# Kernel tuning notes

Hardware: AMD Instinct MI355X
Metric: run time of the kernel (lower is better)

The kernel has to match this reference:

```python
import jax, jax.numpy as jnp
import numpy as np

N = 50000      # nodes
E = 800000     # edges
IN = 256       # in_channels
OUT = 128      # out_channels
HID = 2 * OUT  # hidden = 2*out_channels


def setup_inputs() -> dict:
    key = jax.random.key(0)
    ks = jax.random.split(key, 8)
    x = jax.random.normal(ks[0], (N, IN), dtype=jnp.float32)
    edge_index = jax.random.randint(ks[1], (2, E), 0, N, dtype=jnp.int32)
    def glorot(k, fan_in, fan_out):
        return jax.random.normal(k, (fan_in, fan_out), jnp.float32) * np.float32(1.0 / np.sqrt(fan_in))
    W1 = glorot(ks[2], IN, HID)
    b1 = jnp.zeros((HID,), jnp.float32)
    Wmu = glorot(ks[3], HID, OUT)
    bmu = jnp.zeros((OUT,), jnp.float32)
    Wls = glorot(ks[4], HID, OUT)
    bls = jnp.zeros((OUT,), jnp.float32)
    return {"x": x, "edge_index": edge_index, "W1": W1, "b1": b1,
            "Wmu": Wmu, "bmu": bmu, "Wls": Wls, "bls": bls}


def reference(x, edge_index, W1, b1, Wmu, bmu, Wls, bls):
    n = x.shape[0]
    # add self-loops (PyG GCNConv default add_self_loops=True)
    loop = jnp.arange(n, dtype=edge_index.dtype)
    src = jnp.concatenate([edge_index[0], loop])  # message sources (row)
    dst = jnp.concatenate([edge_index[1], loop])  # aggregation targets (col)
    # symmetric normalization: deg over targets, norm = d^-1/2[src] * d^-1/2[dst]
    deg = jax.ops.segment_sum(jnp.ones(src.shape[0], x.dtype), dst, num_segments=n)
    dinv = jnp.where(deg > 0, jax.lax.rsqrt(deg), 0.0)
    norm = dinv[src] * dinv[dst]  # [E+N]

    def gcn(h, W, b):
        h = h @ W                                   # [N, F_out] dense transform
        msg = h[src] * norm[:, None]                # gather + scale   [E+N, F_out]
        agg = jax.ops.segment_sum(msg, dst, num_segments=n)  # scatter-add
        return agg + b

    h = jax.nn.relu(gcn(x, W1, b1))
    return gcn(h, Wmu, bmu), gcn(h, Wls, bls)
```

## Files before the change

### kernel.cpp

```cpp
#include <hip/hip_runtime.h>
#include <hip/hip_fp16.h>

typedef __attribute__((ext_vector_type(8))) _Float16 half8;
typedef __attribute__((ext_vector_type(4))) _Float16 half4;
typedef __attribute__((ext_vector_type(4))) float float4v;

#define LDP2 72


__global__ __launch_bounds__(256) void k_deg(const int* __restrict__ dst, int* __restrict__ deg, int E) {
    int e = blockIdx.x * 256 + threadIdx.x;
    if (e < E) atomicAdd(&deg[dst[e]], 1);
}


__global__ __launch_bounds__(256) void k_scan1(const int* __restrict__ deg, int* __restrict__ rowptr,
                                               int* __restrict__ bsum, float* __restrict__ dinv, int N) {
    __shared__ int sm[256];
    const int t = threadIdx.x;
    const int i = blockIdx.x * 256 + t;
    int v = (i < N) ? deg[i] : 0;
    if (i < N) dinv[i] = rsqrtf((float)(v + 1));
    int x = v;
    sm[t] = x;
    __syncthreads();
#pragma unroll
    for (int off = 1; off < 256; off <<= 1) {
        int y = (t >= off) ? sm[t - off] : 0;
        __syncthreads();
        x += y;
        sm[t] = x;
        __syncthreads();
    }
    if (i < N) rowptr[i] = x - v;
    if (t == 255) bsum[blockIdx.x] = x;
}

__global__ __launch_bounds__(256) void k_scan2(int* __restrict__ bsum, int* __restrict__ rowptr, int nb, int N) {
    __shared__ int sm[256];
    const int t = threadIdx.x;
    int v = (t < nb) ? bsum[t] : 0;
    int x = v;
    sm[t] = x;
    __syncthreads();
#pragma unroll
    for (int off = 1; off < 256; off <<= 1) {
        int y = (t >= off) ? sm[t - off] : 0;
        __syncthreads();
        x += y;
        sm[t] = x;
        __syncthreads();
    }
    if (t < nb) bsum[t] = x - v;
    if (t == 255) rowptr[N] = x;
}

__global__ __launch_bounds__(256) void k_scan3(int* __restrict__ rowptr, const int* __restrict__ bsum, int N) {
    int i = blockIdx.x * 256 + threadIdx.x;
    if (i < N) rowptr[i] += bsum[blockIdx.x];
}

__global__ __launch_bounds__(256) void k_fill(const int* __restrict__ src, const int* __restrict__ dst,
                                              const int* __restrict__ rowptr, int* __restrict__ rowcnt,
                                              int* __restrict__ csr, int E) {
    int e = blockIdx.x * 256 + threadIdx.x;
    if (e < E) {
        int d = dst[e];
        int pos = rowptr[d] + atomicAdd(&rowcnt[d], 1);
        csr[pos] = src[e];
    }
}

__global__ __launch_bounds__(256) void k_wt(const float* __restrict__ W1, const float* __restrict__ Wmu,
                                            const float* __restrict__ Wls, _Float16* __restrict__ Wt1,
                                            _Float16* __restrict__ Wct) {
    int b = blockIdx.x;
    int t = threadIdx.x;
    if (b < 256) {
        Wt1[b * 256 + t] = (_Float16)W1[t * 256 + b];
    } else {
        int j = b - 256;
        float v = (j < 128) ? Wmu[t * 128 + j] : Wls[t * 128 + (j - 128)];
        Wct[j * 256 + t] = (_Float16)v;
    }
}

template <int AF32, int OUTF32>
__global__ __launch_bounds__(256) void gemm_k(const void* __restrict__ Aptr, const _Float16* __restrict__ Bt,
                                              const float* __restrict__ bmu, const float* __restrict__ bls,
                                              const float* __restrict__ dinv,
                                              void* __restrict__ outp, int M, size_t split) {
    __shared__ _Float16 As[128 * LDP2];
    __shared__ _Float16 Bs[128 * LDP2];
    const int t = threadIdx.x;
    const int lane = t & 63;
    const int wid = t >> 6;
    const int bm = blockIdx.x * 128;
    const int bn = blockIdx.y * 128;
    const int wm = (wid & 1) * 64;
    const int wn = (wid >> 1) * 64;

    float4v acc[4][4];
#pragma unroll
    for (int i = 0; i < 4; i++)
#pragma unroll
        for (int j = 0; j < 4; j++) acc[i][j] = (float4v){0.f, 0.f, 0.f, 0.f};

    float4v ar32[8];
    half8 ar16[4];
    half8 br[4];

    const int a32row = t >> 1;
    const int a32ko = (t & 1) * 32;

    auto load_regs = [&](int kt) {
        if (AF32) {
            const float* A = (const float*)Aptr;
            int gr = bm + a32row; if (gr >= M) gr = M - 1;
            const float4v* p = (const float4v*)(A + (size_t)gr * 256 + kt + a32ko);
#pragma unroll
            for (int q = 0; q < 8; q++) ar32[q] = p[q];
        } else {
            const _Float16* A = (const _Float16*)Aptr;
#pragma unroll
            for (int m = 0; m < 4; m++) {
                int u = m * 256 + t;
                int row = u >> 3, k8 = (u & 7) * 8;
                int gr = bm + row; if (gr >= M) gr = M - 1;
                ar16[m] = *(const half8*)(A + (size_t)gr * 256 + kt + k8);
            }
        }
#pragma unroll
        for (int m = 0; m < 4; m++) {
            int u = m * 256 + t;
            int row = u >> 3, k8 = (u & 7) * 8;
            br[m] = *(const half8*)(Bt + (size_t)(bn + row) * 256 + kt + k8);
        }
    };

    auto write_lds = [&]() {
        if (AF32) {
#pragma unroll
            for (int q = 0; q < 4; q++) {
                half8 h;
#pragma unroll
                for (int j = 0; j < 4; j++) { h[j] = (_Float16)ar32[2 * q][j]; h[4 + j] = (_Float16)ar32[2 * q + 1][j]; }
                *(half8*)&As[a32row * LDP2 + a32ko + q * 8] = h;
            }
        } else {
#pragma unroll
            for (int m = 0; m < 4; m++) {
                int u = m * 256 + t;
                int row = u >> 3, k8 = (u & 7) * 8;
                *(half8*)&As[row * LDP2 + k8] = ar16[m];
            }
        }
#pragma unroll
        for (int m = 0; m < 4; m++) {
            int u = m * 256 + t;
            int row = u >> 3, k8 = (u & 7) * 8;
            *(half8*)&Bs[row * LDP2 + k8] = br[m];
        }
    };

    load_regs(0);
#pragma unroll
    for (int it = 0; it < 4; it++) {
        if (it > 0) __syncthreads();
        write_lds();
        __syncthreads();
        if (it < 3) load_regs((it + 1) * 64);

        const int kg = (lane >> 4) * 8;
        const int fr = lane & 15;
#pragma unroll
        for (int kk = 0; kk < 64; kk += 32) {
            half8 af[4], bf[4];
#pragma unroll
            for (int f = 0; f < 4; f++) af[f] = *(const half8*)&As[(wm + f * 16 + fr) * LDP2 + kk + kg];
#pragma unroll
            for (int f = 0; f < 4; f++) bf[f] = *(const half8*)&Bs[(wn + f * 16 + fr) * LDP2 + kk + kg];
#pragma unroll
            for (int i = 0; i < 4; i++)
#pragma unroll
                for (int j = 0; j < 4; j++)
                    acc[i][j] = __builtin_amdgcn_mfma_f32_16x16x32_f16(af[i], bf[j], acc[i][j], 0, 0, 0);
        }
    }

    const int fc = lane & 15;
    const int rq = (lane >> 4) * 4;
    if (OUTF32) {
        float* out = (float*)outp;
#pragma unroll
        for (int i = 0; i < 4; i++) {
#pragma unroll
            for (int j = 0; j < 4; j++) {
                int col = bn + wn + j * 16 + fc;
                float bias = (col < 128) ? bmu[col] : bls[col - 128];
#pragma unroll
                for (int r = 0; r < 4; r++) {
                    int row = bm + wm + i * 16 + rq + r;
                    if (row < M) {
                        size_t o = (col < 128) ? ((size_t)row * 128 + col)
                                               : (split + (size_t)row * 128 + (col - 128));
                        out[o] = acc[i][j][r] + bias;
                    }
                }
            }
        }
    } else {
        _Float16* out = (_Float16*)outp;
#pragma unroll
        for (int i = 0; i < 4; i++) {
#pragma unroll
            for (int r = 0; r < 4; r++) {
                int row = bm + wm + i * 16 + rq + r;
                if (row < M) {
                    float sc = dinv[row];
#pragma unroll
                    for (int j = 0; j < 4; j++) {
                        int col = bn + wn + j * 16 + fc;
                        out[(size_t)row * 256 + col] = (_Float16)(acc[i][j][r] * sc);
                    }
                }
            }
        }
    }
}

__global__ __launch_bounds__(256) void k_agg(const _Float16* __restrict__ in, _Float16* __restrict__ out,
                                             const float* __restrict__ dinv, const int* __restrict__ rowptr,
                                             const int* __restrict__ csr, const float* __restrict__ bias,
                                             int mode, int N) {
    const int g = blockIdx.x * 4 + (threadIdx.x >> 6);
    const int lane = threadIdx.x & 63;
    if (g >= N) return;
    const float dd = dinv[g];
    const int beg = rowptr[g], end = rowptr[g + 1];
    const size_t fo = (size_t)lane * 4;

    float acc[4];
    {
        half4 hv = *(const half4*)(in + (size_t)g * 256 + fo);
#pragma unroll
        for (int j = 0; j < 4; j++) acc[j] = (float)hv[j];
    }
    int e = beg;
    for (; e + 4 <= end; e += 4) {
        int s0 = csr[e], s1 = csr[e + 1], s2 = csr[e + 2], s3 = csr[e + 3];
        half4 v0 = *(const half4*)(in + (size_t)s0 * 256 + fo);
        half4 v1 = *(const half4*)(in + (size_t)s1 * 256 + fo);
        half4 v2 = *(const half4*)(in + (size_t)s2 * 256 + fo);
        half4 v3 = *(const half4*)(in + (size_t)s3 * 256 + fo);
#pragma unroll
        for (int j = 0; j < 4; j++)
            acc[j] += (float)v0[j] + (float)v1[j] + (float)v2[j] + (float)v3[j];
    }
    for (; e < end; ++e) {
        int s = csr[e];
        half4 v = *(const half4*)(in + (size_t)s * 256 + fo);
#pragma unroll
        for (int j = 0; j < 4; j++) acc[j] += (float)v[j];
    }

    half4 o;
    if (mode) {
#pragma unroll
        for (int j = 0; j < 4; j++) {
            float r = fmaxf(acc[j] * dd + bias[lane * 4 + j], 0.f);
            o[j] = (_Float16)(r * dd);
        }
    } else {
#pragma unroll
        for (int j = 0; j < 4; j++) o[j] = (_Float16)(acc[j] * dd);
    }
    *(half4*)(out + (size_t)g * 256 + fo) = o;
}


extern "C" void kernel_launch(void* const* d_in, const int* in_sizes, int n_in,
                              void* d_out, int out_size, void* d_ws, size_t ws_size,
                              hipStream_t stream) {
    const float* x   = (const float*)d_in[0];
    const int*   ei  = (const int*)d_in[1];
    const float* W1  = (const float*)d_in[2];
    const float* b1  = (const float*)d_in[3];
    const float* Wmu = (const float*)d_in[4];
    const float* bmu = (const float*)d_in[5];
    const float* Wls = (const float*)d_in[6];
    const float* bls = (const float*)d_in[7];
    const int N = in_sizes[0] / 256;
    const int E = in_sizes[1] / 2;
    const int* esrc = ei;
    const int* edst = ei + E;

    char* ws = (char*)d_ws;
    size_t off = 0;
    auto alloc = [&](size_t bytes) -> void* {
        void* p = ws + off;
        off += (bytes + 255) & ~(size_t)255;
        return p;
    };
    _Float16* h1  = (_Float16*)alloc((size_t)N * 256 * 2);
    _Float16* hb  = (_Float16*)alloc((size_t)N * 256 * 2);
    _Float16* Wt1 = (_Float16*)alloc(256 * 256 * 2);
    _Float16* Wct = (_Float16*)alloc(256 * 256 * 2);
    float* dinv   = (float*)alloc((size_t)N * 4);
    int* degcnt   = (int*)alloc((size_t)N * 2 * 4);
    int* deg      = degcnt;
    int* rowcnt   = degcnt + N;
    int* rowptr   = (int*)alloc((size_t)(N + 1) * 4);
    int* bsum     = (int*)alloc(256 * 4);
    int* csr      = (int*)alloc((size_t)E * 4);

    const int nb = (N + 255) / 256;

    hipMemsetAsync(degcnt, 0, (size_t)N * 2 * 4, stream);

    k_deg<<<(E + 255) / 256, 256, 0, stream>>>(edst, deg, E);
    k_scan1<<<nb, 256, 0, stream>>>(deg, rowptr, bsum, dinv, N);
    k_scan2<<<1, 256, 0, stream>>>(bsum, rowptr, nb, N);
    k_scan3<<<nb, 256, 0, stream>>>(rowptr, bsum, N);
    k_fill<<<(E + 255) / 256, 256, 0, stream>>>(esrc, edst, rowptr, rowcnt, csr, E);
    k_wt<<<512, 256, 0, stream>>>(W1, Wmu, Wls, Wt1, Wct);

    dim3 gg((N + 127) / 128, 2);
    gemm_k<1, 0><<<gg, 256, 0, stream>>>(x, Wt1, nullptr, nullptr, dinv, h1, N, 0);
    k_agg<<<(N + 3) / 4, 256, 0, stream>>>(h1, hb, dinv, rowptr, csr, b1, 1, N);
    k_agg<<<(N + 3) / 4, 256, 0, stream>>>(hb, h1, dinv, rowptr, csr, nullptr, 0, N);
    gemm_k<0, 1><<<gg, 256, 0, stream>>>(h1, Wct, bmu, bls, nullptr, d_out, N, (size_t)N * 128);
}
```

Measured before the change: 360.7 us.

## Remap GEMM tiles per XCD and split aggregation edges across half-waves

```diff
diff --git a/kernel.cpp b/kernel.cpp
--- a/kernel.cpp
+++ b/kernel.cpp
@@ -95,8 +95,15 @@
     const int t = threadIdx.x;
     const int lane = t & 63;
     const int wid = t >> 6;
-    const int bm = blockIdx.x * 128;
-    const int bn = blockIdx.y * 128;
+
+    const int nwg = gridDim.x;
+    const int wg = blockIdx.x;
+    const int q8 = nwg >> 3, r8 = nwg & 7;
+    const int xcd = wg & 7, pos = wg >> 3;
+    const int v = (xcd < r8) ? (xcd * (q8 + 1) + pos) : (r8 * (q8 + 1) + (xcd - r8) * q8 + pos);
+    const int bm = (v >> 1) * 128;
+    const int bn = (v & 1) * 128;
+
     const int wm = (wid & 1) * 64;
     const int wn = (wid >> 1) * 64;
 
@@ -229,53 +236,84 @@
     }
 }
 
-__global__ __launch_bounds__(256) void k_agg(const _Float16* __restrict__ in, _Float16* __restrict__ out,
+__global__ __launch_bounds__(128) void k_agg(const _Float16* __restrict__ in, _Float16* __restrict__ out,
                                              const float* __restrict__ dinv, const int* __restrict__ rowptr,
                                              const int* __restrict__ csr, const float* __restrict__ bias,
                                              int mode, int N) {
-    const int g = blockIdx.x * 4 + (threadIdx.x >> 6);
+    const int g = blockIdx.x * 2 + (threadIdx.x >> 6);
+    if (g >= N) return;
     const int lane = threadIdx.x & 63;
-    if (g >= N) return;
-    const float dd = dinv[g];
+    const int half = lane >> 5;
+    const int fl = lane & 31;
+    const size_t fo = (size_t)fl * 8;
+    const _Float16* __restrict__ base = in + fo;
+
     const int beg = rowptr[g], end = rowptr[g + 1];
-    const size_t fo = (size_t)lane * 4;
-
-    float acc[4];
-    {
-        half4 hv = *(const half4*)(in + (size_t)g * 256 + fo);
-#pragma unroll
-        for (int j = 0; j < 4; j++) acc[j] = (float)hv[j];
-    }
-    int e = beg;
-    for (; e + 4 <= end; e += 4) {
-        int s0 = csr[e], s1 = csr[e + 1], s2 = csr[e + 2], s3 = csr[e + 3];
-        half4 v0 = *(const half4*)(in + (size_t)s0 * 256 + fo);
-        half4 v1 = *(const half4*)(in + (size_t)s1 * 256 + fo);
-        half4 v2 = *(const half4*)(in + (size_t)s2 * 256 + fo);
-        half4 v3 = *(const half4*)(in + (size_t)s3 * 256 + fo);
-#pragma unroll
-        for (int j = 0; j < 4; j++)
-            acc[j] += (float)v0[j] + (float)v1[j] + (float)v2[j] + (float)v3[j];
-    }
-    for (; e < end; ++e) {
+    const int nq = (end - beg) >> 2;
+
+    float acc[8];
+    if (half == 0) {
+        half8 sv = *(const half8*)(base + (size_t)g * 256);
+#pragma unroll
+        for (int j = 0; j < 8; j++) acc[j] = (float)sv[j];
+    } else {
+#pragma unroll
+        for (int j = 0; j < 8; j++) acc[j] = 0.f;
+    }
+
+    int p = beg + half;
+    half8 va, vb;
+    if (nq > 0) {
+        int ia = csr[p], ib = csr[p + 2];
+        va = *(const half8*)(base + (size_t)ia * 256);
+        vb = *(const half8*)(base + (size_t)ib * 256);
+    }
+    for (int q = 0; q + 1 < nq; q++) {
+        int na = csr[p + 4], nb = csr[p + 6];
+        half8 wa = *(const half8*)(base + (size_t)na * 256);
+        half8 wb = *(const half8*)(base + (size_t)nb * 256);
+#pragma unroll
+        for (int j = 0; j < 8; j++) acc[j] += (float)va[j];
+#pragma unroll
+        for (int j = 0; j < 8; j++) acc[j] += (float)vb[j];
+        va = wa; vb = wb;
+        p += 4;
+    }
+    if (nq > 0) {
+#pragma unroll
+        for (int j = 0; j < 8; j++) acc[j] += (float)va[j];
+#pragma unroll
+        for (int j = 0; j < 8; j++) acc[j] += (float)vb[j];
+    }
+    for (int e = beg + 4 * nq + half; e < end; e += 2) {
         int s = csr[e];
-        half4 v = *(const half4*)(in + (size_t)s * 256 + fo);
-#pragma unroll
-        for (int j = 0; j < 4; j++) acc[j] += (float)v[j];
-    }
-
-    half4 o;
-    if (mode) {
-#pragma unroll
-        for (int j = 0; j < 4; j++) {
-            float r = fmaxf(acc[j] * dd + bias[lane * 4 + j], 0.f);
-            o[j] = (_Float16)(r * dd);
-        }
-    } else {
-#pragma unroll
-        for (int j = 0; j < 4; j++) o[j] = (_Float16)(acc[j] * dd);
-    }
-    *(half4*)(out + (size_t)g * 256 + fo) = o;
+        half8 v = *(const half8*)(base + (size_t)s * 256);
+#pragma unroll
+        for (int j = 0; j < 8; j++) acc[j] += (float)v[j];
+    }
+
+#pragma unroll
+    for (int j = 0; j < 8; j++) acc[j] += __shfl_xor(acc[j], 32);
+
+    if (half == 0) {
+        const float dd = dinv[g];
+        half8 o;
+        if (mode) {
+            const float4v* bp = (const float4v*)(bias + fl * 8);
+            float4v b0 = bp[0], b1 = bp[1];
+#pragma unroll
+            for (int j = 0; j < 4; j++) {
+                float r0 = fmaxf(acc[j] * dd + b0[j], 0.f);
+                o[j] = (_Float16)(r0 * dd);
+                float r1 = fmaxf(acc[4 + j] * dd + b1[j], 0.f);
+                o[4 + j] = (_Float16)(r1 * dd);
+            }
+        } else {
+#pragma unroll
+            for (int j = 0; j < 8; j++) o[j] = (_Float16)(acc[j] * dd);
+        }
+        *(half8*)(out + (size_t)g * 256 + fo) = o;
+    }
 }
 
 
@@ -325,9 +363,9 @@
     k_fill<<<(E + 255) / 256, 256, 0, stream>>>(esrc, edst, rowptr, rowcnt, csr, E);
     k_wt<<<512, 256, 0, stream>>>(W1, Wmu, Wls, Wt1, Wct);
 
-    dim3 gg((N + 127) / 128, 2);
-    gemm_k<1, 0><<<gg, 256, 0, stream>>>(x, Wt1, nullptr, nullptr, dinv, h1, N, 0);
-    k_agg<<<(N + 3) / 4, 256, 0, stream>>>(h1, hb, dinv, rowptr, csr, b1, 1, N);
-    k_agg<<<(N + 3) / 4, 256, 0, stream>>>(hb, h1, dinv, rowptr, csr, nullptr, 0, N);
-    gemm_k<0, 1><<<gg, 256, 0, stream>>>(h1, Wct, bmu, bls, nullptr, d_out, N, (size_t)N * 128);
-}
+    const int nbm = (N + 127) / 128;
+    gemm_k<1, 0><<<nbm * 2, 256, 0, stream>>>(x, Wt1, nullptr, nullptr, dinv, h1, N, 0);
+    k_agg<<<(N + 1) / 2, 128, 0, stream>>>(h1, hb, dinv, rowptr, csr, b1, 1, N);
+    k_agg<<<(N + 1) / 2, 128, 0, stream>>>(hb, h1, dinv, rowptr, csr, nullptr, 0, N);
+    gemm_k<0, 1><<<nbm * 2, 256, 0, stream>>>(h1, Wct, bmu, bls, nullptr, d_out, N, (size_t)N * 128);
+}
```

Measured after the change: 357.0 us. No clear change (-1.0%).

## Tile hidden features into 32-wide column slabs and remap blocks per XCD

Applied to the files above, without the earlier changes.

```diff
diff --git a/kernel.cpp b/kernel.cpp
--- a/kernel.cpp
+++ b/kernel.cpp
@@ -3,6 +3,7 @@
 
 typedef __attribute__((ext_vector_type(8))) _Float16 half8;
 typedef __attribute__((ext_vector_type(4))) _Float16 half4;
+typedef __attribute__((ext_vector_type(2))) _Float16 half2v;
 typedef __attribute__((ext_vector_type(4))) float float4v;
 
 #define LDP2 72
@@ -95,8 +96,15 @@
     const int t = threadIdx.x;
     const int lane = t & 63;
     const int wid = t >> 6;
-    const int bm = blockIdx.x * 128;
-    const int bn = blockIdx.y * 128;
+
+    const int nwg = gridDim.x;
+    const int wg = blockIdx.x;
+    const int q8 = nwg >> 3, r8 = nwg & 7;
+    const int xcd = wg & 7, pos = wg >> 3;
+    const int v = (xcd < r8) ? (xcd * (q8 + 1) + pos) : (r8 * (q8 + 1) + (xcd - r8) * q8 + pos);
+    const int bm = (v >> 1) * 128;
+    const int bn = (v & 1) * 128;
+
     const int wm = (wid & 1) * 64;
     const int wn = (wid >> 1) * 64;
 
@@ -127,7 +135,8 @@
                 int u = m * 256 + t;
                 int row = u >> 3, k8 = (u & 7) * 8;
                 int gr = bm + row; if (gr >= M) gr = M - 1;
-                ar16[m] = *(const half8*)(A + (size_t)gr * 256 + kt + k8);
+                int k = kt + k8;
+                ar16[m] = *(const half8*)(A + (size_t)(k >> 5) * M * 32 + (size_t)gr * 32 + (k & 31));
             }
         }
 #pragma unroll
@@ -221,7 +230,8 @@
 #pragma unroll
                     for (int j = 0; j < 4; j++) {
                         int col = bn + wn + j * 16 + fc;
-                        out[(size_t)row * 256 + col] = (_Float16)(acc[i][j][r] * sc);
+                        out[(size_t)(col >> 5) * M * 32 + (size_t)row * 32 + (col & 31)] =
+                            (_Float16)(acc[i][j][r] * sc);
                     }
                 }
             }
@@ -229,53 +239,47 @@
     }
 }
 
-__global__ __launch_bounds__(256) void k_agg(const _Float16* __restrict__ in, _Float16* __restrict__ out,
-                                             const float* __restrict__ dinv, const int* __restrict__ rowptr,
-                                             const int* __restrict__ csr, const float* __restrict__ bias,
-                                             int mode, int N) {
-    const int g = blockIdx.x * 4 + (threadIdx.x >> 6);
+template <int MODE>
+__global__ __launch_bounds__(256) void k_agg_t(const _Float16* __restrict__ in, _Float16* __restrict__ out,
+                                               const float* __restrict__ dinv, const int* __restrict__ rowptr,
+                                               const int* __restrict__ csr, const float* __restrict__ bias,
+                                               int N) {
+    const int tile = blockIdx.x & 7;
+    const int g = (blockIdx.x >> 3) * 4 + (threadIdx.x >> 6);
+    if (g >= N) return;
     const int lane = threadIdx.x & 63;
-    if (g >= N) return;
-    const float dd = dinv[g];
+    const int eg = lane >> 4;
+    const int fl = lane & 15;
+    const _Float16* __restrict__ tin = in + (size_t)tile * N * 32;
+
     const int beg = rowptr[g], end = rowptr[g + 1];
-    const size_t fo = (size_t)lane * 4;
-
-    float acc[4];
-    {
-        half4 hv = *(const half4*)(in + (size_t)g * 256 + fo);
-#pragma unroll
-        for (int j = 0; j < 4; j++) acc[j] = (float)hv[j];
-    }
-    int e = beg;
-    for (; e + 4 <= end; e += 4) {
-        int s0 = csr[e], s1 = csr[e + 1], s2 = csr[e + 2], s3 = csr[e + 3];
-        half4 v0 = *(const half4*)(in + (size_t)s0 * 256 + fo);
-        half4 v1 = *(const half4*)(in + (size_t)s1 * 256 + fo);
-        half4 v2 = *(const half4*)(in + (size_t)s2 * 256 + fo);
-        half4 v3 = *(const half4*)(in + (size_t)s3 * 256 + fo);
-#pragma unroll
-        for (int j = 0; j < 4; j++)
-            acc[j] += (float)v0[j] + (float)v1[j] + (float)v2[j] + (float)v3[j];
-    }
-    for (; e < end; ++e) {
+    float a0 = 0.f, a1 = 0.f;
+    for (int e = beg + eg; e < end; e += 4) {
         int s = csr[e];
-        half4 v = *(const half4*)(in + (size_t)s * 256 + fo);
-#pragma unroll
-        for (int j = 0; j < 4; j++) acc[j] += (float)v[j];
-    }
-
-    half4 o;
-    if (mode) {
-#pragma unroll
-        for (int j = 0; j < 4; j++) {
-            float r = fmaxf(acc[j] * dd + bias[lane * 4 + j], 0.f);
-            o[j] = (_Float16)(r * dd);
-        }
-    } else {
-#pragma unroll
-        for (int j = 0; j < 4; j++) o[j] = (_Float16)(acc[j] * dd);
-    }
-    *(half4*)(out + (size_t)g * 256 + fo) = o;
+        half2v v = *(const half2v*)(tin + (size_t)s * 32 + fl * 2);
+        a0 += (float)v[0];
+        a1 += (float)v[1];
+    }
+    a0 += __shfl_xor(a0, 16); a0 += __shfl_xor(a0, 32);
+    a1 += __shfl_xor(a1, 16); a1 += __shfl_xor(a1, 32);
+
+    if (eg == 0) {
+        half2v sv = *(const half2v*)(tin + (size_t)g * 32 + fl * 2);
+        a0 += (float)sv[0];
+        a1 += (float)sv[1];
+        const float dd = dinv[g];
+        half2v o;
+        if (MODE) {
+            float b0 = bias[tile * 32 + fl * 2];
+            float b1 = bias[tile * 32 + fl * 2 + 1];
+            o[0] = (_Float16)(fmaxf(a0 * dd + b0, 0.f) * dd);
+            o[1] = (_Float16)(fmaxf(a1 * dd + b1, 0.f) * dd);
+        } else {
+            o[0] = (_Float16)(a0 * dd);
+            o[1] = (_Float16)(a1 * dd);
+        }
+        *(half2v*)(out + (size_t)tile * N * 32 + (size_t)g * 32 + fl * 2) = o;
+    }
 }
 
 
@@ -325,9 +329,10 @@
     k_fill<<<(E + 255) / 256, 256, 0, stream>>>(esrc, edst, rowptr, rowcnt, csr, E);
     k_wt<<<512, 256, 0, stream>>>(W1, Wmu, Wls, Wt1, Wct);
 
-    dim3 gg((N + 127) / 128, 2);
-    gemm_k<1, 0><<<gg, 256, 0, stream>>>(x, Wt1, nullptr, nullptr, dinv, h1, N, 0);
-    k_agg<<<(N + 3) / 4, 256, 0, stream>>>(h1, hb, dinv, rowptr, csr, b1, 1, N);
-    k_agg<<<(N + 3) / 4, 256, 0, stream>>>(hb, h1, dinv, rowptr, csr, nullptr, 0, N);
-    gemm_k<0, 1><<<gg, 256, 0, stream>>>(h1, Wct, bmu, bls, nullptr, d_out, N, (size_t)N * 128);
-}
+    const int nbm = (N + 127) / 128;
+    const int nba = 8 * ((N + 3) / 4);
+    gemm_k<1, 0><<<nbm * 2, 256, 0, stream>>>(x, Wt1, nullptr, nullptr, dinv, h1, N, 0);
+    k_agg_t<1><<<nba, 256, 0, stream>>>(h1, hb, dinv, rowptr, csr, b1, N);
+    k_agg_t<0><<<nba, 256, 0, stream>>>(hb, h1, dinv, rowptr, csr, nullptr, N);
+    gemm_k<0, 1><<<nbm * 2, 256, 0, stream>>>(h1, Wct, bmu, bls, nullptr, d_out, N, (size_t)N * 128);
+}
```

Result: slower. 548.2 us (+52.0%).
